# Performance work log

Measured on AMD Instinct MI355X. Metric: run time of the kernel, lower is better.

The kernel has to match this reference:

```python
import jax, jax.numpy as jnp
import numpy as np

N_BATCHES = 32
N_LABELS = 100


def setup_inputs() -> dict:
    key = jax.random.key(0)
    ks = jax.random.split(key, 7)
    N, D, P = 16384, 2048, 256
    x = jax.random.normal(ks[0], (N, D), dtype=jnp.float32)
    label = jax.random.randint(ks[1], (N,), 0, N_LABELS, dtype=jnp.int64)
    label_batch = jnp.sort(jax.random.randint(ks[2], (N,), 0, N_BATCHES, dtype=jnp.int64))
    W1_w = jax.random.normal(ks[3], (P, D), dtype=jnp.float32) * 0.02
    W1_b = jax.random.normal(ks[4], (P,), dtype=jnp.float32) * 0.02
    W2_w = jax.random.normal(ks[5], (P, D), dtype=jnp.float32) * 0.02
    W2_b = jax.random.normal(ks[6], (P,), dtype=jnp.float32) * 0.02
    return {"x": x, "label": label, "label_batch": label_batch,
            "W1_w": W1_w, "W1_b": W1_b, "W2_w": W2_w, "W2_b": W2_b}


def _loo_diff_label_mean(x, label, label_batch):
    # For each sample i: mean of x over {j : label_batch[j]==label_batch[i] and label[j]!=label[i]}.
    # Rows with no such j are zero (torch code's `continue`). x is detached in the original.
    N = x.shape[0]
    xs = jax.lax.stop_gradient(x)
    seg = label_batch * N_LABELS + label                      # combined (group,label) key
    n_seg = N_BATCHES * N_LABELS
    ones = jnp.ones((N,), dtype=x.dtype)
    sum_bl = jax.ops.segment_sum(xs, seg, num_segments=n_seg)            # [n_seg, D]
    cnt_bl = jax.ops.segment_sum(ones, seg, num_segments=n_seg)          # [n_seg]
    sum_b = jax.ops.segment_sum(xs, label_batch, num_segments=N_BATCHES)  # [NB, D]
    cnt_b = jax.ops.segment_sum(ones, label_batch, num_segments=N_BATCHES)
    diff_sum = sum_b[label_batch] - sum_bl[seg]               # [N, D]
    diff_cnt = cnt_b[label_batch] - cnt_bl[seg]               # [N]
    safe = jnp.maximum(diff_cnt, 1.0)
    mean = diff_sum / safe[:, None]
    return jnp.where((diff_cnt > 0)[:, None], mean, jnp.zeros_like(mean))


def reference(x, label, label_batch, W1_w, W1_b, W2_w, W2_b):
    calc_mean = _loo_diff_label_mean(x, label, label_batch)   # detached aggregate
    return x @ W1_w.T + W1_b + calc_mean @ W2_w.T + W2_b      # W1(x) + W2(mean)
```

## Files before the change

### kernel.cpp

```cpp
#include <hip/hip_runtime.h>
#include <cstdint>

#define N_SAMPLES 16384
#define DIM 2048
#define PDIM 256
#define NB 32
#define NL 100
#define NSEG (NB * NL)

typedef float floatx4 __attribute__((ext_vector_type(4)));
typedef __bf16 bf16x8 __attribute__((ext_vector_type(8)));

__device__ __forceinline__ unsigned short f32_to_bf16(float f) {
    unsigned int u = __float_as_uint(f);
    u += 0x7fffu + ((u >> 16) & 1u);
    return (unsigned short)(u >> 16);
}
__device__ __forceinline__ unsigned int pack_bf16x2(float a, float b) {
    return (unsigned int)f32_to_bf16(a) | ((unsigned int)f32_to_bf16(b) << 16);
}

__global__ __launch_bounds__(256) void prep_kernel(
    const float* __restrict__ W1w, const float* __restrict__ W1b,
    const float* __restrict__ W2w, const float* __restrict__ W2b,
    const int* __restrict__ label, const int* __restrict__ lbatch,
    unsigned short* __restrict__ W1bf, unsigned short* __restrict__ W2bf,
    float* __restrict__ bias, int* __restrict__ seg,
    int* __restrict__ hist, float* __restrict__ SW2)
{
    int i = blockIdx.x * 256 + threadIdx.x;
    W1bf[i] = f32_to_bf16(W1w[i]);
    W2bf[i] = f32_to_bf16(W2w[i]);
    if (i < PDIM) bias[i] = W1b[i] + W2b[i];
    if (i < N_SAMPLES) seg[i] = lbatch[i] * NL + label[i];
    if (i < NSEG) hist[i] = 0;
    if (i < NSEG * PDIM / 2) ((float2*)SW2)[i] = make_float2(0.f, 0.f);
}

__global__ __launch_bounds__(256) void hist_kernel(
    const int* __restrict__ seg, int* __restrict__ hist)
{
    int i = blockIdx.x * 256 + threadIdx.x;
    atomicAdd(&hist[seg[i]], 1);
}

#define SCAN_BPT 13
__global__ __launch_bounds__(256) void scan_kernel(
    const int* __restrict__ hist, int* __restrict__ offs, int* __restrict__ cursor)
{
    __shared__ int ps[256];
    const int t = threadIdx.x;
    int local = 0;
    #pragma unroll
    for (int k = 0; k < SCAN_BPT; ++k) {
        int bin = t * SCAN_BPT + k;
        if (bin < NSEG) local += hist[bin];
    }
    ps[t] = local;
    __syncthreads();
    for (int d = 1; d < 256; d <<= 1) {
        int v = (t >= d) ? ps[t - d] : 0;
        __syncthreads();
        ps[t] += v;
        __syncthreads();
    }
    int run = ps[t] - local;
    #pragma unroll
    for (int k = 0; k < SCAN_BPT; ++k) {
        int bin = t * SCAN_BPT + k;
        if (bin < NSEG) {
            offs[bin] = run;
            cursor[bin] = run;
            run += hist[bin];
        }
    }
    if (t == 255) offs[NSEG] = ps[255];
}

__global__ __launch_bounds__(256) void scatter_kernel(
    const int* __restrict__ seg, int* __restrict__ cursor, int* __restrict__ perm)
{
    int i = blockIdx.x * 256 + threadIdx.x;
    int pos = atomicAdd(&cursor[seg[i]], 1);
    perm[pos] = i;
}

__global__ __launch_bounds__(256) void segsum_kernel(
    const float* __restrict__ x, const int* __restrict__ perm,
    const int* __restrict__ offs,
    unsigned short* __restrict__ xb, unsigned short* __restrict__ sumb)
{
    const int tid = threadIdx.x;
    const int w = tid >> 6, lane = tid & 63;
    const int s = blockIdx.y * 4 + w;
    const int c = blockIdx.x * 512 + lane * 8;
    const int beg = offs[s], end = offs[s + 1];

    floatx4 sum0 = {0.f, 0.f, 0.f, 0.f};
    floatx4 sum1 = {0.f, 0.f, 0.f, 0.f};
    for (int base = beg; base < end; base += 64) {
        int p = (base + lane < end) ? perm[base + lane] : 0;
        const int n = min(end - base, 64);
        for (int j0 = 0; j0 < n; j0 += 8) {
            int rr[8];
            floatx4 v0[8], v1[8];
            #pragma unroll
            for (int j = 0; j < 8; ++j) {
                rr[j] = __shfl(p, min(j0 + j, n - 1));
                const float* px = &x[(size_t)rr[j] * DIM + c];
                v0[j] = *(const floatx4*)px;
                v1[j] = *(const floatx4*)(px + 4);
            }
            #pragma unroll
            for (int j = 0; j < 8; ++j) {
                if (j < n - j0) {
                    sum0 += v0[j];
                    sum1 += v1[j];
                    uint4 o;
                    o.x = pack_bf16x2(v0[j][0], v0[j][1]);
                    o.y = pack_bf16x2(v0[j][2], v0[j][3]);
                    o.z = pack_bf16x2(v1[j][0], v1[j][1]);
                    o.w = pack_bf16x2(v1[j][2], v1[j][3]);
                    *(uint4*)&xb[(size_t)rr[j] * DIM + c] = o;
                }
            }
        }
    }
    uint4 so;
    so.x = pack_bf16x2(sum0[0], sum0[1]);
    so.y = pack_bf16x2(sum0[2], sum0[3]);
    so.z = pack_bf16x2(sum1[0], sum1[1]);
    so.w = pack_bf16x2(sum1[2], sum1[3]);
    *(uint4*)&sumb[(size_t)s * DIM + c] = so;
}

__global__ __launch_bounds__(256) void finalize_kernel(
    float* __restrict__ SW2, const int* __restrict__ offs)
{
    const int b = blockIdx.x;
    const int col = threadIdx.x;
    const int cb = offs[(b + 1) * NL] - offs[b * NL];
    float tot = 0.f;
    #pragma unroll 4
    for (int l = 0; l < NL; ++l)
        tot += SW2[(size_t)(b * NL + l) * PDIM + col];
    for (int l = 0; l < NL; ++l) {
        const int s = b * NL + l;
        const int dc = cb - (offs[s + 1] - offs[s]);
        const float v = SW2[(size_t)s * PDIM + col];
        SW2[(size_t)s * PDIM + col] = (dc > 0) ? (tot - v) / (float)dc : 0.f;
    }
}

template<int BM, int BN, int WR, int WC, bool FUSE, int KSPLIT>
__global__ __launch_bounds__(256) void gemm_bt_kernel(
    const unsigned short* __restrict__ A,
    const unsigned short* __restrict__ B,
    float* __restrict__ C,
    const float* __restrict__ bias,
    const float* __restrict__ add,
    const int* __restrict__ seg,
    int K)
{
    constexpr int SM = BM / WR, SN = BN / WC;
    constexpr int FM = SM / 16, FN = SN / 16;
    __shared__ __align__(16) unsigned short ldsA[BM * 32];
    __shared__ __align__(16) unsigned short ldsB[BN * 32];
    const int tid = threadIdx.x;
    const int lane = tid & 63;
    const int wave = tid >> 6;
    const int wr = wave / WC, wc = wave % WC;
    const int quad = lane >> 4, l15 = lane & 15;
    const int m0 = blockIdx.x * BM;
    const int n0 = blockIdx.y * BN;
    const int kpw = K / KSPLIT;
    const int k0 = blockIdx.z * kpw;
    const int srow = lane >> 2, schunk = lane & 3;

    floatx4 acc[FM][FN];
    #pragma unroll
    for (int i = 0; i < FM; ++i)
        #pragma unroll
        for (int j = 0; j < FN; ++j) acc[i][j] = (floatx4){0.f, 0.f, 0.f, 0.f};

    const unsigned short* Abase = A + (size_t)(m0 + srow) * K + schunk * 8;
    const unsigned short* Bbase = B + (size_t)(n0 + srow) * K + schunk * 8;

    for (int kk = k0; kk < k0 + kpw; kk += 32) {
        __syncthreads();
        #pragma unroll
        for (int ch = wave; ch < BM / 16; ch += 4)
            __builtin_amdgcn_global_load_lds(
                (const __attribute__((address_space(1))) void*)(Abase + (size_t)ch * 16 * K + kk),
                (__attribute__((address_space(3))) void*)&ldsA[ch * 16 * 32], 16, 0, 0);
        #pragma unroll
        for (int ch = wave; ch < BN / 16; ch += 4)
            __builtin_amdgcn_global_load_lds(
                (const __attribute__((address_space(1))) void*)(Bbase + (size_t)ch * 16 * K + kk),
                (__attribute__((address_space(3))) void*)&ldsB[ch * 16 * 32], 16, 0, 0);
        __syncthreads();

        bf16x8 af[FM], bfr[FN];
        #pragma unroll
        for (int mi = 0; mi < FM; ++mi)
            af[mi] = *(const bf16x8*)&ldsA[(wr * SM + mi * 16 + l15) * 32 + quad * 8];
        #pragma unroll
        for (int ni = 0; ni < FN; ++ni)
            bfr[ni] = *(const bf16x8*)&ldsB[(wc * SN + ni * 16 + l15) * 32 + quad * 8];
        #pragma unroll
        for (int mi = 0; mi < FM; ++mi)
            #pragma unroll
            for (int ni = 0; ni < FN; ++ni)
                acc[mi][ni] = __builtin_amdgcn_mfma_f32_16x16x32_bf16(
                    af[mi], bfr[ni], acc[mi][ni], 0, 0, 0);
    }

    #pragma unroll
    for (int mi = 0; mi < FM; ++mi) {
        const int rbase = m0 + wr * SM + mi * 16 + quad * 4;
        #pragma unroll
        for (int ni = 0; ni < FN; ++ni) {
            const int col = n0 + wc * SN + ni * 16 + l15;
            float bsum = 0.f;
            if constexpr (FUSE) bsum = bias[col];
            #pragma unroll
            for (int r = 0; r < 4; ++r) {
                const int row = rbase + r;
                float v = acc[mi][ni][r];
                if constexpr (FUSE) v += bsum + add[(size_t)seg[row] * PDIM + col];
                if constexpr (KSPLIT > 1)
                    atomicAdd(&C[(size_t)row * PDIM + col], v);
                else
                    C[(size_t)row * PDIM + col] = v;
            }
        }
    }
}

extern "C" void kernel_launch(void* const* d_in, const int* in_sizes, int n_in,
                              void* d_out, int out_size, void* d_ws, size_t ws_size,
                              hipStream_t stream)
{
    const float* x      = (const float*)d_in[0];
    const int*   label  = (const int*)d_in[1];
    const int*   lbatch = (const int*)d_in[2];
    const float* W1w    = (const float*)d_in[3];
    const float* W1b    = (const float*)d_in[4];
    const float* W2w    = (const float*)d_in[5];
    const float* W2b    = (const float*)d_in[6];
    float* out = (float*)d_out;

    char* ws = (char*)d_ws;
    size_t off = 0;
    auto alloc = [&](size_t bytes) {
        void* p = ws + off;
        off = (off + bytes + 255) & ~(size_t)255;
        return p;
    };
    unsigned short* xb   = (unsigned short*)alloc((size_t)N_SAMPLES * DIM * 2);
    unsigned short* sumb = (unsigned short*)alloc((size_t)NSEG * DIM * 2);
    unsigned short* W1bf = (unsigned short*)alloc((size_t)PDIM * DIM * 2);
    unsigned short* W2bf = (unsigned short*)alloc((size_t)PDIM * DIM * 2);
    float* SW2    = (float*)alloc((size_t)NSEG * PDIM * 4);
    float* bias   = (float*)alloc(PDIM * 4);
    int*   seg    = (int*)alloc(N_SAMPLES * 4);
    int*   perm   = (int*)alloc(N_SAMPLES * 4);
    int*   hist   = (int*)alloc(NSEG * 4);
    int*   offs   = (int*)alloc((NSEG + 1) * 4);
    int*   cursor = (int*)alloc(NSEG * 4);

    prep_kernel<<<PDIM * DIM / 256, 256, 0, stream>>>(
        W1w, W1b, W2w, W2b, label, lbatch, W1bf, W2bf, bias, seg, hist, SW2);

    hist_kernel<<<N_SAMPLES / 256, 256, 0, stream>>>(seg, hist);
    scan_kernel<<<1, 256, 0, stream>>>(hist, offs, cursor);
    scatter_kernel<<<N_SAMPLES / 256, 256, 0, stream>>>(seg, cursor, perm);

    segsum_kernel<<<dim3(DIM / 512, NSEG / 4), 256, 0, stream>>>(
        x, perm, offs, xb, sumb);

    gemm_bt_kernel<32, 256, 1, 4, false, 2>
        <<<dim3(NSEG / 32, 1, 2), 256, 0, stream>>>(
        sumb, W2bf, SW2, nullptr, nullptr, nullptr, DIM);

    finalize_kernel<<<NB, 256, 0, stream>>>(SW2, offs);

    gemm_bt_kernel<64, 128, 2, 2, true, 1>
        <<<dim3(N_SAMPLES / 64, PDIM / 128), 256, 0, stream>>>(
        xb, W1bf, out, bias, SW2, seg, DIM);
}
```

Baseline: 316.3 us.

## Replace segment-sum pipeline with single fused GEMM projecting x through W1 and W2

Result: faster. 298.1 us (-5.8%).

```diff
diff --git a/kernel.cpp b/kernel.cpp
--- a/kernel.cpp
+++ b/kernel.cpp
@@ -24,217 +24,146 @@
     const float* __restrict__ W1w, const float* __restrict__ W1b,
     const float* __restrict__ W2w, const float* __restrict__ W2b,
     const int* __restrict__ label, const int* __restrict__ lbatch,
-    unsigned short* __restrict__ W1bf, unsigned short* __restrict__ W2bf,
-    float* __restrict__ bias, int* __restrict__ seg,
-    int* __restrict__ hist, float* __restrict__ SW2)
+    unsigned short* __restrict__ Wbf, float* __restrict__ bias,
+    int* __restrict__ seg, int* __restrict__ cnt, float* __restrict__ SW2)
 {
     int i = blockIdx.x * 256 + threadIdx.x;
-    W1bf[i] = f32_to_bf16(W1w[i]);
-    W2bf[i] = f32_to_bf16(W2w[i]);
+    Wbf[i]              = f32_to_bf16(W1w[i]);
+    Wbf[PDIM * DIM + i] = f32_to_bf16(W2w[i]);
     if (i < PDIM) bias[i] = W1b[i] + W2b[i];
     if (i < N_SAMPLES) seg[i] = lbatch[i] * NL + label[i];
-    if (i < NSEG) hist[i] = 0;
+    if (i < NSEG) cnt[i] = 0;
     if (i < NSEG * PDIM / 2) ((float2*)SW2)[i] = make_float2(0.f, 0.f);
 }
 
 __global__ __launch_bounds__(256) void hist_kernel(
-    const int* __restrict__ seg, int* __restrict__ hist)
+    const int* __restrict__ seg, int* __restrict__ cnt)
 {
     int i = blockIdx.x * 256 + threadIdx.x;
-    atomicAdd(&hist[seg[i]], 1);
-}
-
-#define SCAN_BPT 13
-__global__ __launch_bounds__(256) void scan_kernel(
-    const int* __restrict__ hist, int* __restrict__ offs, int* __restrict__ cursor)
-{
-    __shared__ int ps[256];
-    const int t = threadIdx.x;
-    int local = 0;
+    atomicAdd(&cnt[seg[i]], 1);
+}
+
+__global__ __launch_bounds__(256) void gemm_fused_kernel(
+    const float* __restrict__ x, const unsigned short* __restrict__ Wbf,
+    const float* __restrict__ bias, const int* __restrict__ seg,
+    float* __restrict__ out, float* __restrict__ SW2)
+{
+    constexpr int BM = 64, BN = 256, BK = 32;
+    __shared__ __align__(16) unsigned short ldsA[BM * BK];
+    __shared__ __align__(16) unsigned short ldsB[BN * BK];
+    const int tid = threadIdx.x;
+    const int lane = tid & 63;
+    const int wave = tid >> 6;
+    const int quad = lane >> 4, l15 = lane & 15;
+    const int nhalf = blockIdx.x;
+    const int m0 = blockIdx.y * BM;
+    const int srow = lane >> 2, schunk = lane & 3;
+    const int arow = tid >> 2;
+    const int akc = (tid & 3) * 8;
+
+    floatx4 acc[4][4];
     #pragma unroll
-    for (int k = 0; k < SCAN_BPT; ++k) {
-        int bin = t * SCAN_BPT + k;
-        if (bin < NSEG) local += hist[bin];
+    for (int i = 0; i < 4; ++i)
+        #pragma unroll
+        for (int j = 0; j < 4; ++j) acc[i][j] = (floatx4){0.f, 0.f, 0.f, 0.f};
+
+    const float* Ax = x + (size_t)(m0 + arow) * DIM + akc;
+    const unsigned short* Bbase =
+        Wbf + ((size_t)(nhalf * BN) + srow) * DIM + schunk * 8;
+
+    for (int kk = 0; kk < DIM; kk += BK) {
+        float4 a0 = *(const float4*)(Ax + kk);
+        float4 a1 = *(const float4*)(Ax + kk + 4);
+        __syncthreads();
+        uint4 ao;
+        ao.x = pack_bf16x2(a0.x, a0.y);
+        ao.y = pack_bf16x2(a0.z, a0.w);
+        ao.z = pack_bf16x2(a1.x, a1.y);
+        ao.w = pack_bf16x2(a1.z, a1.w);
+        *(uint4*)&ldsA[arow * BK + akc] = ao;
+        #pragma unroll
+        for (int ch = wave; ch < BN / 16; ch += 4)
+            __builtin_amdgcn_global_load_lds(
+                (const __attribute__((address_space(1))) void*)(Bbase + (size_t)ch * 16 * DIM + kk),
+                (__attribute__((address_space(3))) void*)&ldsB[ch * 16 * BK], 16, 0, 0);
+        __syncthreads();
+
+        bf16x8 af[4], bf[4];
+        #pragma unroll
+        for (int mi = 0; mi < 4; ++mi)
+            af[mi] = *(const bf16x8*)&ldsA[(mi * 16 + l15) * BK + quad * 8];
+        #pragma unroll
+        for (int ni = 0; ni < 4; ++ni)
+            bf[ni] = *(const bf16x8*)&ldsB[(wave * 64 + ni * 16 + l15) * BK + quad * 8];
+        #pragma unroll
+        for (int mi = 0; mi < 4; ++mi)
+            #pragma unroll
+            for (int ni = 0; ni < 4; ++ni)
+                acc[mi][ni] = __builtin_amdgcn_mfma_f32_16x16x32_bf16(
+                    af[mi], bf[ni], acc[mi][ni], 0, 0, 0);
     }
-    ps[t] = local;
-    __syncthreads();
-    for (int d = 1; d < 256; d <<= 1) {
-        int v = (t >= d) ? ps[t - d] : 0;
-        __syncthreads();
-        ps[t] += v;
-        __syncthreads();
-    }
-    int run = ps[t] - local;
-    #pragma unroll
-    for (int k = 0; k < SCAN_BPT; ++k) {
-        int bin = t * SCAN_BPT + k;
-        if (bin < NSEG) {
-            offs[bin] = run;
-            cursor[bin] = run;
-            run += hist[bin];
+
+    if (nhalf == 0) {
+        #pragma unroll
+        for (int mi = 0; mi < 4; ++mi) {
+            const int rbase = m0 + mi * 16 + quad * 4;
+            #pragma unroll
+            for (int ni = 0; ni < 4; ++ni) {
+                const int col = wave * 64 + ni * 16 + l15;
+                const float bs = bias[col];
+                #pragma unroll
+                for (int r = 0; r < 4; ++r)
+                    out[(size_t)(rbase + r) * PDIM + col] = acc[mi][ni][r] + bs;
+            }
         }
-    }
-    if (t == 255) offs[NSEG] = ps[255];
-}
-
-__global__ __launch_bounds__(256) void scatter_kernel(
-    const int* __restrict__ seg, int* __restrict__ cursor, int* __restrict__ perm)
-{
-    int i = blockIdx.x * 256 + threadIdx.x;
-    int pos = atomicAdd(&cursor[seg[i]], 1);
-    perm[pos] = i;
-}
-
-__global__ __launch_bounds__(256) void segsum_kernel(
-    const float* __restrict__ x, const int* __restrict__ perm,
-    const int* __restrict__ offs,
-    unsigned short* __restrict__ xb, unsigned short* __restrict__ sumb)
-{
-    const int tid = threadIdx.x;
-    const int w = tid >> 6, lane = tid & 63;
-    const int s = blockIdx.y * 4 + w;
-    const int c = blockIdx.x * 512 + lane * 8;
-    const int beg = offs[s], end = offs[s + 1];
-
-    floatx4 sum0 = {0.f, 0.f, 0.f, 0.f};
-    floatx4 sum1 = {0.f, 0.f, 0.f, 0.f};
-    for (int base = beg; base < end; base += 64) {
-        int p = (base + lane < end) ? perm[base + lane] : 0;
-        const int n = min(end - base, 64);
-        for (int j0 = 0; j0 < n; j0 += 8) {
-            int rr[8];
-            floatx4 v0[8], v1[8];
+    } else {
+        #pragma unroll
+        for (int mi = 0; mi < 4; ++mi) {
+            const int rbase = m0 + mi * 16 + quad * 4;
             #pragma unroll
-            for (int j = 0; j < 8; ++j) {
-                rr[j] = __shfl(p, min(j0 + j, n - 1));
-                const float* px = &x[(size_t)rr[j] * DIM + c];
-                v0[j] = *(const floatx4*)px;
-                v1[j] = *(const floatx4*)(px + 4);
-            }
-            #pragma unroll
-            for (int j = 0; j < 8; ++j) {
-                if (j < n - j0) {
-                    sum0 += v0[j];
-                    sum1 += v1[j];
-                    uint4 o;
-                    o.x = pack_bf16x2(v0[j][0], v0[j][1]);
-                    o.y = pack_bf16x2(v0[j][2], v0[j][3]);
-                    o.z = pack_bf16x2(v1[j][0], v1[j][1]);
-                    o.w = pack_bf16x2(v1[j][2], v1[j][3]);
-                    *(uint4*)&xb[(size_t)rr[j] * DIM + c] = o;
+            for (int r = 0; r < 4; ++r) {
+                const int sr = seg[rbase + r];
+                #pragma unroll
+                for (int ni = 0; ni < 4; ++ni) {
+                    const int col = wave * 64 + ni * 16 + l15;
+                    atomicAdd(&SW2[(size_t)sr * PDIM + col], acc[mi][ni][r]);
                 }
             }
         }
     }
-    uint4 so;
-    so.x = pack_bf16x2(sum0[0], sum0[1]);
-    so.y = pack_bf16x2(sum0[2], sum0[3]);
-    so.z = pack_bf16x2(sum1[0], sum1[1]);
-    so.w = pack_bf16x2(sum1[2], sum1[3]);
-    *(uint4*)&sumb[(size_t)s * DIM + c] = so;
 }
 
 __global__ __launch_bounds__(256) void finalize_kernel(
-    float* __restrict__ SW2, const int* __restrict__ offs)
+    float* __restrict__ SW2, const int* __restrict__ cnt)
 {
     const int b = blockIdx.x;
     const int col = threadIdx.x;
-    const int cb = offs[(b + 1) * NL] - offs[b * NL];
+    int cb = 0;
+    #pragma unroll 4
+    for (int l = 0; l < NL; ++l) cb += cnt[b * NL + l];
     float tot = 0.f;
     #pragma unroll 4
     for (int l = 0; l < NL; ++l)
         tot += SW2[(size_t)(b * NL + l) * PDIM + col];
     for (int l = 0; l < NL; ++l) {
         const int s = b * NL + l;
-        const int dc = cb - (offs[s + 1] - offs[s]);
+        const int dc = cb - cnt[s];
         const float v = SW2[(size_t)s * PDIM + col];
         SW2[(size_t)s * PDIM + col] = (dc > 0) ? (tot - v) / (float)dc : 0.f;
     }
 }
 
-template<int BM, int BN, int WR, int WC, bool FUSE, int KSPLIT>
-__global__ __launch_bounds__(256) void gemm_bt_kernel(
-    const unsigned short* __restrict__ A,
-    const unsigned short* __restrict__ B,
-    float* __restrict__ C,
-    const float* __restrict__ bias,
-    const float* __restrict__ add,
-    const int* __restrict__ seg,
-    int K)
-{
-    constexpr int SM = BM / WR, SN = BN / WC;
-    constexpr int FM = SM / 16, FN = SN / 16;
-    __shared__ __align__(16) unsigned short ldsA[BM * 32];
-    __shared__ __align__(16) unsigned short ldsB[BN * 32];
-    const int tid = threadIdx.x;
-    const int lane = tid & 63;
-    const int wave = tid >> 6;
-    const int wr = wave / WC, wc = wave % WC;
-    const int quad = lane >> 4, l15 = lane & 15;
-    const int m0 = blockIdx.x * BM;
-    const int n0 = blockIdx.y * BN;
-    const int kpw = K / KSPLIT;
-    const int k0 = blockIdx.z * kpw;
-    const int srow = lane >> 2, schunk = lane & 3;
-
-    floatx4 acc[FM][FN];
-    #pragma unroll
-    for (int i = 0; i < FM; ++i)
-        #pragma unroll
-        for (int j = 0; j < FN; ++j) acc[i][j] = (floatx4){0.f, 0.f, 0.f, 0.f};
-
-    const unsigned short* Abase = A + (size_t)(m0 + srow) * K + schunk * 8;
-    const unsigned short* Bbase = B + (size_t)(n0 + srow) * K + schunk * 8;
-
-    for (int kk = k0; kk < k0 + kpw; kk += 32) {
-        __syncthreads();
-        #pragma unroll
-        for (int ch = wave; ch < BM / 16; ch += 4)
-            __builtin_amdgcn_global_load_lds(
-                (const __attribute__((address_space(1))) void*)(Abase + (size_t)ch * 16 * K + kk),
-                (__attribute__((address_space(3))) void*)&ldsA[ch * 16 * 32], 16, 0, 0);
-        #pragma unroll
-        for (int ch = wave; ch < BN / 16; ch += 4)
-            __builtin_amdgcn_global_load_lds(
-                (const __attribute__((address_space(1))) void*)(Bbase + (size_t)ch * 16 * K + kk),
-                (__attribute__((address_space(3))) void*)&ldsB[ch * 16 * 32], 16, 0, 0);
-        __syncthreads();
-
-        bf16x8 af[FM], bfr[FN];
-        #pragma unroll
-        for (int mi = 0; mi < FM; ++mi)
-            af[mi] = *(const bf16x8*)&ldsA[(wr * SM + mi * 16 + l15) * 32 + quad * 8];
-        #pragma unroll
-        for (int ni = 0; ni < FN; ++ni)
-            bfr[ni] = *(const bf16x8*)&ldsB[(wc * SN + ni * 16 + l15) * 32 + quad * 8];
-        #pragma unroll
-        for (int mi = 0; mi < FM; ++mi)
-            #pragma unroll
-            for (int ni = 0; ni < FN; ++ni)
-                acc[mi][ni] = __builtin_amdgcn_mfma_f32_16x16x32_bf16(
-                    af[mi], bfr[ni], acc[mi][ni], 0, 0, 0);
-    }
-
-    #pragma unroll
-    for (int mi = 0; mi < FM; ++mi) {
-        const int rbase = m0 + wr * SM + mi * 16 + quad * 4;
-        #pragma unroll
-        for (int ni = 0; ni < FN; ++ni) {
-            const int col = n0 + wc * SN + ni * 16 + l15;
-            float bsum = 0.f;
-            if constexpr (FUSE) bsum = bias[col];
-            #pragma unroll
-            for (int r = 0; r < 4; ++r) {
-                const int row = rbase + r;
-                float v = acc[mi][ni][r];
-                if constexpr (FUSE) v += bsum + add[(size_t)seg[row] * PDIM + col];
-                if constexpr (KSPLIT > 1)
-                    atomicAdd(&C[(size_t)row * PDIM + col], v);
-                else
-                    C[(size_t)row * PDIM + col] = v;
-            }
-        }
-    }
+__global__ __launch_bounds__(256) void epilogue_kernel(
+    float* __restrict__ out, const float* __restrict__ SW2,
+    const int* __restrict__ seg)
+{
+    const int idx = blockIdx.x * 256 + threadIdx.x;
+    const int row = idx >> 6;
+    const int c = (idx & 63) * 4;
+    float4 v = ((const float4*)out)[idx];
+    const float4 s4 = *(const float4*)&SW2[(size_t)seg[row] * PDIM + c];
+    v.x += s4.x; v.y += s4.y; v.z += s4.z; v.w += s4.w;
+    ((float4*)out)[idx] = v;
 }
 
 extern "C" void kernel_launch(void* const* d_in, const int* in_sizes, int n_in,
@@ -257,35 +186,22 @@
         off = (off + bytes + 255) & ~(size_t)255;
         return p;
     };
-    unsigned short* xb   = (unsigned short*)alloc((size_t)N_SAMPLES * DIM * 2);
-    unsigned short* sumb = (unsigned short*)alloc((size_t)NSEG * DIM * 2);
-    unsigned short* W1bf = (unsigned short*)alloc((size_t)PDIM * DIM * 2);
-    unsigned short* W2bf = (unsigned short*)alloc((size_t)PDIM * DIM * 2);
-    float* SW2    = (float*)alloc((size_t)NSEG * PDIM * 4);
-    float* bias   = (float*)alloc(PDIM * 4);
-    int*   seg    = (int*)alloc(N_SAMPLES * 4);
-    int*   perm   = (int*)alloc(N_SAMPLES * 4);
-    int*   hist   = (int*)alloc(NSEG * 4);
-    int*   offs   = (int*)alloc((NSEG + 1) * 4);
-    int*   cursor = (int*)alloc(NSEG * 4);
+    unsigned short* Wbf = (unsigned short*)alloc((size_t)2 * PDIM * DIM * 2);
+    float* SW2  = (float*)alloc((size_t)NSEG * PDIM * 4);
+    float* bias = (float*)alloc(PDIM * 4);
+    int*   seg  = (int*)alloc(N_SAMPLES * 4);
+    int*   cnt  = (int*)alloc(NSEG * 4);
 
     prep_kernel<<<PDIM * DIM / 256, 256, 0, stream>>>(
-        W1w, W1b, W2w, W2b, label, lbatch, W1bf, W2bf, bias, seg, hist, SW2);
-
-    hist_kernel<<<N_SAMPLES / 256, 256, 0, stream>>>(seg, hist);
-    scan_kernel<<<1, 256, 0, stream>>>(hist, offs, cursor);
-    scatter_kernel<<<N_SAMPLES / 256, 256, 0, stream>>>(seg, cursor, perm);
-
-    segsum_kernel<<<dim3(DIM / 512, NSEG / 4), 256, 0, stream>>>(
-        x, perm, offs, xb, sumb);
-
-    gemm_bt_kernel<32, 256, 1, 4, false, 2>
-        <<<dim3(NSEG / 32, 1, 2), 256, 0, stream>>>(
-        sumb, W2bf, SW2, nullptr, nullptr, nullptr, DIM);
-
-    finalize_kernel<<<NB, 256, 0, stream>>>(SW2, offs);
-
-    gemm_bt_kernel<64, 128, 2, 2, true, 1>
-        <<<dim3(N_SAMPLES / 64, PDIM / 128), 256, 0, stream>>>(
-        xb, W1bf, out, bias, SW2, seg, DIM);
-}
+        W1w, W1b, W2w, W2b, label, lbatch, Wbf, bias, seg, cnt, SW2);
+
+    hist_kernel<<<N_SAMPLES / 256, 256, 0, stream>>>(seg, cnt);
+
+    gemm_fused_kernel<<<dim3(2, N_SAMPLES / 64), 256, 0, stream>>>(
+        x, Wbf, bias, seg, out, SW2);
+
+    finalize_kernel<<<NB, 256, 0, stream>>>(SW2, cnt);
+
+    epilogue_kernel<<<(size_t)N_SAMPLES * PDIM / 4 / 256, 256, 0, stream>>>(
+        out, SW2, seg);
+}
```
